# Kernel optimization log

Measured on AMD Instinct MI355X. Metric: run time of the kernel, lower is better.

The kernel has to match this reference:

```python
import jax, jax.numpy as jnp
import numpy as np

B, C, H, W = 2, 16, 128, 128
PS = (3, 5, 7)
N_BG, N_TG = 64, 8


def _unfold(x, p):
    # torch F.unfold(kernel=p, padding=p//2, stride=1): [B,C,H,W] -> [B, C*p*p, H*W]
    pad = p // 2
    b, c, h, w = x.shape
    xp = jnp.pad(x, ((0, 0), (0, 0), (pad, pad), (pad, pad)))
    # channel-major, then kernel row, kernel col (torch layout)
    pat = jnp.stack([xp[:, :, i:i + h, j:j + w] for i in range(p) for j in range(p)], axis=2)
    return pat.reshape(b, c * p * p, h * w)


def _fold(cols, p, h, w):
    # torch F.fold(output_size=(h,w), kernel=p, padding=p//2, stride=1): overlap-add scatter
    b, d, _ = cols.shape
    c = d // (p * p)
    pad = p // 2
    pat = cols.reshape(b, c, p * p, h, w)
    canvas = jnp.zeros((b, c, h + 2 * pad, w + 2 * pad), cols.dtype)
    for k in range(p * p):
        i, j = divmod(k, p)
        canvas = canvas.at[:, :, i:i + h, j:j + w].add(pat[:, :, k])
    return canvas[:, :, pad:pad + h, pad:pad + w]


def _branch(x, memory, temp, p):
    # _read_memory ('dot' similarity) + fold reconstruction with overlap-count divisor
    b, c, h, w = x.shape
    d = memory.shape[1]  # c*p*p
    xu = _unfold(x, p).transpose(0, 2, 1)                      # [B, HW, D]
    sim = jnp.einsum('bld,md->blm', xu, memory) * (temp[0] / d ** 0.5)
    att = jax.nn.softmax(sim, axis=2)                          # [B, HW, M]
    read = jnp.einsum('blm,md->bld', att, memory)              # [B, HW, D]
    out_sum = _fold(read.transpose(0, 2, 1), p, h, w)
    ones = jnp.ones((1, 1, h, w), x.dtype)
    div = _fold(_unfold(ones, p), p, h, w)                     # overlap counts
    return out_sum / (div + 1e-8)


def _fusion(feats, w1, b1, w2, b2):
    # MultiScaleFusion, fusion_type='attention'
    n = len(feats)
    b, c = feats[0].shape[0], feats[0].shape[1]
    u = feats[0]
    for f in feats[1:]:
        u = u + f
    pooled = u.mean(axis=(2, 3))                               # [B, C]
    hdn = jax.nn.relu(pooled @ w1.T + b1)                      # [B, C//4]
    logits = (hdn @ w2.T + b2).reshape(b, n, c)                # [B, n, C]
    wt = jax.nn.softmax(logits, axis=1)[..., None, None]       # softmax over scales
    return (jnp.stack(feats, axis=1) * wt).sum(axis=1)


def setup_inputs() -> dict:
    key = jax.random.key(0)
    ks = jax.random.split(key, 20)
    inp = {
        'bg': jax.random.normal(ks[0], (B, C, H, W), jnp.float32),
        'tg': jax.random.normal(ks[1], (B, C, H, W), jnp.float32),
    }
    for i, p in enumerate(PS):
        inp[f'bg_mem{i}'] = jax.random.normal(ks[2 + i], (N_BG, C * p * p), jnp.float32)
        inp[f'tg_mem{i}'] = jax.random.normal(ks[5 + i], (N_TG, C * p * p), jnp.float32)
        inp[f'bg_temp{i}'] = jnp.full((1,), 10.0, jnp.float32)
        inp[f'tg_temp{i}'] = jnp.full((1,), 10.0, jnp.float32)
    hid = C // 4
    n = len(PS)
    s1 = (1.0 / C) ** 0.5
    s2 = (1.0 / hid) ** 0.5
    inp['bg_fc1_w'] = jax.random.uniform(ks[8], (hid, C), jnp.float32, -s1, s1)
    inp['bg_fc1_b'] = jax.random.uniform(ks[9], (hid,), jnp.float32, -s1, s1)
    inp['bg_fc2_w'] = jax.random.uniform(ks[10], (C * n, hid), jnp.float32, -s2, s2)
    inp['bg_fc2_b'] = jax.random.uniform(ks[11], (C * n,), jnp.float32, -s2, s2)
    inp['tg_fc1_w'] = jax.random.uniform(ks[12], (hid, C), jnp.float32, -s1, s1)
    inp['tg_fc1_b'] = jax.random.uniform(ks[13], (hid,), jnp.float32, -s1, s1)
    inp['tg_fc2_w'] = jax.random.uniform(ks[14], (C * n, hid), jnp.float32, -s2, s2)
    inp['tg_fc2_b'] = jax.random.uniform(ks[15], (C * n,), jnp.float32, -s2, s2)
    return inp


def reference(bg, tg,
              bg_mem0, bg_mem1, bg_mem2, bg_temp0, bg_temp1, bg_temp2,
              tg_mem0, tg_mem1, tg_mem2, tg_temp0, tg_temp1, tg_temp2,
              bg_fc1_w, bg_fc1_b, bg_fc2_w, bg_fc2_b,
              tg_fc1_w, tg_fc1_b, tg_fc2_w, tg_fc2_b):
    bg_feats = [_branch(bg, m, t, p) for m, t, p in
                zip((bg_mem0, bg_mem1, bg_mem2), (bg_temp0, bg_temp1, bg_temp2), PS)]
    f_bc = _fusion(bg_feats, bg_fc1_w, bg_fc1_b, bg_fc2_w, bg_fc2_b)
    tg_feats = [_branch(tg, m, t, p) for m, t, p in
                zip((tg_mem0, tg_mem1, tg_mem2), (tg_temp0, tg_temp1, tg_temp2), PS)]
    f_tg = _fusion(tg_feats, tg_fc1_w, tg_fc1_b, tg_fc2_w, tg_fc2_b)
    return (f_bc, f_tg)
```

## Files before the change

kernel.cpp:

```cpp
#include <hip/hip_runtime.h>

#define C_CH 16
#define Hdim 128
#define Wdim 128
#define HWdim 16384
#define CHW (C_CH * HWdim)
#define Bdim 2
#define PAIR_ELEMS (Bdim * CHW)

#define XWP 140
#define XHP 140
#define XPL (XHP * XWP)

typedef float v2f __attribute__((ext_vector_type(2)));
typedef _Float16 h2 __attribute__((ext_vector_type(2)));
typedef _Float16 f16x8 __attribute__((ext_vector_type(8)));
typedef float f32x4 __attribute__((ext_vector_type(4)));

__device__ __forceinline__ unsigned pack2(float a, float b) {
  h2 h = {(_Float16)a, (_Float16)b};
  return __builtin_bit_cast(unsigned, h);
}
__device__ __forceinline__ void gadd(float* p, float v) {
  __hip_atomic_fetch_add(p, v, __ATOMIC_RELAXED, __HIP_MEMORY_SCOPE_AGENT);
}

struct PrepDesc {
  const float* mem;
  const float* temp;
  _Float16* simA;
  _Float16* readA;
  int M, D, P, tg;
};
struct PrepArgs { PrepDesc d[6]; };

__global__ __launch_bounds__(256) void k_preppad(PrepArgs a,
                                                 const float* __restrict__ bg,
                                                 const float* __restrict__ tg,
                                                 unsigned* __restrict__ xpad2)
{
  int bid = blockIdx.x;
  if (bid < 2048) {
    int idx = bid * 256 + threadIdx.x;
    int pp = idx >> 14;
    int hw = idx & (HWdim - 1);
    int y = hw >> 7, x = hw & 127;
    int z = pp >> 3, cp = pp & 7;
    const float* src = (z < 2) ? bg : tg;
    int b = z & 1;
    float av = src[((b * C_CH + 2 * cp) << 14) + hw];
    float bv = src[((b * C_CH + 2 * cp + 1) << 14) + hw];
    xpad2[(size_t)pp * XPL + (y + 6) * XWP + (x + 6)] = pack2(av, bv);
    return;
  }
  int p = bid - 2048;
  int gy = p / 196, gx = p - gy * 196;
  PrepDesc de = a.d[gy];
  int n = de.M * de.D;
  int idx = gx * 256 + threadIdx.x;
  if (idx >= n) return;
  int m = idx / de.D;
  int d = idx - m * de.D;
  float val = de.mem[idx];
  float sc = de.temp[0] / sqrtf((float)de.D);
  int pp = de.P * de.P;
  int c = d / pp;
  int r = d - c * pp;
  int i = r / de.P;
  int j = r - i * de.P;
  int uv = i * de.P + j;
  int uvp = uv >> 1, luv = uv & 1;
  int kk = luv * 16 + c, kg = kk >> 3, kl = kk & 7;
  int u = de.P - 1 - i, v = de.P - 1 - j;
  int uvf = u * de.P + v;
  float sv = val * sc;
  if (!de.tg) {
    int mt = m >> 4, row = m & 15;
    _Float16 hi = (_Float16)sv;
    size_t bi = ((size_t)uvp * 8 + mt) * 512 + row * 32 +
                (size_t)((kg ^ (row & 3)) * 8 + kl);
    de.simA[bi] = hi;
    de.simA[bi + 2048] = (_Float16)(sv - (float)hi);
    int ck = m >> 5, m5 = m & 31, kg2 = m5 >> 3, kl2 = m5 & 7;
    _Float16 hr = (_Float16)val;
    size_t b2 = (size_t)uvf * 2048 + (size_t)(ck * 2) * 512 + c * 32 +
                (size_t)((kg2 ^ (c & 3)) * 8 + kl2);
    de.readA[b2] = hr;
    de.readA[b2 + 512] = (_Float16)(val - (float)hr);
  } else {
    _Float16 hi = (_Float16)sv;
    size_t bi = (size_t)(uvp * 2) * 512 + m * 32 +
                (size_t)((kg ^ (m & 3)) * 8 + kl);
    de.simA[bi] = hi;
    de.simA[bi + 512] = (_Float16)(sv - (float)hi);
    int ch = uvf >> 2, q = uvf & 3;
    _Float16 hr = (_Float16)val;
    size_t b2 = (size_t)ch * 1024 + c * 32 +
                (size_t)((q ^ (c & 3)) * 8 + (m & 7));
    de.readA[b2] = hr;
    de.readA[b2 + 512] = (_Float16)(val - (float)hr);
  }
}

struct FusedArgs {
  const unsigned* xpad2;
  const _Float16* simA[3];
  const _Float16* readA[3];
  const _Float16* simAtg[3];
  const _Float16* readAtg[3];
  float* fbgs[3];
  float* ftgs[3];
  float* pooled;
};

#define SDB_OFF 17920
#define RBUF_OFF 40960
#define FX_SMEM 49152

template<int P, bool BG>
__device__ __forceinline__ void fused_body(
    const unsigned* __restrict__ xp,
    const _Float16* __restrict__ simA,
    const _Float16* __restrict__ readA,
    float* __restrict__ fout,
    float* __restrict__ poolp,
    unsigned char* smem, int tid, int x0, int y0)
{
  constexpr int PAD = P / 2;
  constexpr int THY = 8 + 2 * PAD, THX = 16 + 2 * PAD;
  constexpr int XH = 8 + 4 * PAD, XW = 16 + 4 * PAD;
  constexpr int NXP = XH * XW, NHP = THY * THX;
  constexpr int NT = (NHP + 15) / 16;
  constexpr int NUVP = (P * P + 1) / 2;
  constexpr int NCH = BG ? (P * P + 1) / 2 : (P * P + 3) / 4;
  constexpr int NMT = BG ? 4 : 1;
  constexpr int SCHB = BG ? 8192 : 2048;
  constexpr int RCHB = BG ? 8192 : 2048;
  constexpr int SLD = SCHB / 16, RLD = RCHB / 16;
  constexpr int NRACC = BG ? 4 : 2;

  unsigned char* xbuf = smem;
  unsigned char* att  = smem;
  unsigned char* sdb  = smem + SDB_OFF;
  unsigned char* rbuf = smem + RBUF_OFF;

  const int w = __builtin_amdgcn_readfirstlane(tid >> 6);
  const int lane = tid & 63;
  const int col = lane & 15, g = lane >> 4;

  const int oy = y0 - 2 * PAD + 6, ox = x0 - 2 * PAD + 6;
  for (int t = tid; t < 2 * NXP; t += 512) {
    int h = (t >= NXP) ? 1 : 0;
    int pix = t - h * NXP;
    int ly = pix / XW, lx = pix - ly * XW;
    const unsigned* s = xp + (size_t)(h * 4) * XPL + (oy + ly) * XWP + (ox + lx);
    uint4 vv = { s[0], s[XPL], s[2 * XPL], s[3 * XPL] };
    *(uint4*)(xbuf + (h * NXP + pix) * 16) = vv;
  }

  int ayv[3], axv[3];
#pragma unroll
  for (int ti = 0; ti < 3; ++ti) {
    int nt = w + ti * 8;
    int pix = nt * 16 + col;
    if (pix > NHP - 1) pix = NHP - 1;
    ayv[ti] = pix / THX;
    axv[ti] = pix - ayv[ti] * THX;
  }

  f32x4 acc[3][NMT];
#pragma unroll
  for (int ti = 0; ti < 3; ++ti)
#pragma unroll
    for (int mt = 0; mt < NMT; ++mt) acc[ti][mt] = (f32x4){0.f, 0.f, 0.f, 0.f};

  uint4 sreg;
  if (tid < SLD) sreg = *((const uint4*)simA + tid);
  for (int uvp = 0; uvp < NUVP; ++uvp) {
    if (tid < SLD) {
      *((uint4*)(sdb + (uvp & 1) * SCHB) + tid) = sreg;
      if (uvp + 1 < NUVP)
        sreg = *((const uint4*)(simA + (size_t)(uvp + 1) * (SCHB / 2)) + tid);
    }
    __syncthreads();

    const unsigned char* ab = sdb + (uvp & 1) * SCHB;
    f16x8 af[2][NMT];
#pragma unroll
    for (int s = 0; s < 2; ++s)
#pragma unroll
      for (int mt = 0; mt < NMT; ++mt)
        af[s][mt] = *(const f16x8*)(ab + (s * NMT + mt) * 1024 + col * 64 +
                                    ((g ^ (col & 3)) << 4));

    int uva = 2 * uvp;
    int uvb = uva + 1; if (uvb >= P * P) uvb = uva;
    const int ua = uva / P, va = uva - ua * P;
    const int ub = uvb / P, vb = uvb - ub * P;
    const int u_ = (g >= 2) ? ub : ua;
    const int v_ = (g >= 2) ? vb : va;

#pragma unroll
    for (int ti = 0; ti < 3; ++ti) {
      int nt = w + ti * 8;
      if (nt < NT) {
        int xpix = (ayv[ti] + u_) * XW + axv[ti] + v_;
        f16x8 bb = *(const f16x8*)(xbuf + ((g & 1) * NXP + xpix) * 16);
#pragma unroll
        for (int mt = 0; mt < NMT; ++mt) {
          acc[ti][mt] = __builtin_amdgcn_mfma_f32_16x16x32_f16(af[0][mt], bb, acc[ti][mt], 0, 0, 0);
          acc[ti][mt] = __builtin_amdgcn_mfma_f32_16x16x32_f16(af[1][mt], bb, acc[ti][mt], 0, 0, 0);
        }
      }
    }
  }

  uint4 rreg;
  if (tid < RLD) rreg = *((const uint4*)readA + tid);
  __syncthreads();

#pragma unroll
  for (int ti = 0; ti < 3; ++ti) {
    int nt = w + ti * 8;
    if (nt < NT) {
      int pa = nt * 16 + col;
      int say = pa / THX, sax = pa - say * THX;
      int gy = y0 + say - PAD, gx = x0 + sax - PAD;
      bool inimg = (pa < NHP) & (gy >= 0) & (gy < Hdim) & (gx >= 0) & (gx < Wdim);
      if constexpr (BG) {
        float l[16];
#pragma unroll
        for (int mt = 0; mt < 4; ++mt)
#pragma unroll
          for (int r = 0; r < 4; ++r) l[mt * 4 + r] = acc[ti][mt][r];
        float mx = l[0];
#pragma unroll
        for (int i2 = 1; i2 < 16; ++i2) mx = fmaxf(mx, l[i2]);
        mx = fmaxf(mx, __shfl_xor(mx, 16));
        mx = fmaxf(mx, __shfl_xor(mx, 32));
        float sum = 0.f;
#pragma unroll
        for (int i2 = 0; i2 < 16; ++i2) { l[i2] = __expf(l[i2] - mx); sum += l[i2]; }
        sum += __shfl_xor(sum, 16);
        sum += __shfl_xor(sum, 32);
        float inv = inimg ? (1.f / sum) : 0.f;
        unsigned char* base = att + pa * 128;
        int swz = (pa & 7) << 4;
#pragma unroll
        for (int mt = 0; mt < 4; ++mt) {
          uint2 st = { pack2(l[mt * 4 + 0] * inv, l[mt * 4 + 1] * inv),
                       pack2(l[mt * 4 + 2] * inv, l[mt * 4 + 3] * inv) };
          *(uint2*)(base + ((mt * 32 + g * 8) ^ swz)) = st;
        }
      } else {
        float l0 = acc[ti][0][0], l1 = acc[ti][0][1];
        float l2 = acc[ti][0][2], l3 = acc[ti][0][3];
        float mx = fmaxf(fmaxf(l0, l1), fmaxf(l2, l3));
        mx = fmaxf(mx, __shfl_xor(mx, 16));
        l0 = __expf(l0 - mx); l1 = __expf(l1 - mx);
        l2 = __expf(l2 - mx); l3 = __expf(l3 - mx);
        float sum = l0 + l1 + l2 + l3;
        sum += __shfl_xor(sum, 16);
        float inv = inimg ? (1.f / sum) : 0.f;
        if (g < 2) {
          uint2 st = { pack2(l0 * inv, l1 * inv), pack2(l2 * inv, l3 * inv) };
          *(uint2*)(att + pa * 16 + g * 8) = st;
        }
      }
    }
  }

  f32x4 racc[NRACC];
#pragma unroll
  for (int q = 0; q < NRACC; ++q) racc[q] = (f32x4){0.f, 0.f, 0.f, 0.f};

  for (int ch = 0; ch < NCH; ++ch) {
    __syncthreads();
    if (tid < RLD) {
      *((uint4*)rbuf + tid) = rreg;
      if (ch + 1 < NCH)
        rreg = *((const uint4*)(readA + (size_t)(ch + 1) * (RCHB / 2)) + tid);
    }
    __syncthreads();
    const unsigned char* ab = rbuf;
    if constexpr (BG) {
#pragma unroll
      for (int l = 0; l < 2; ++l) {
        int uv = 2 * ch + l;
        int uvc = (uv > P * P - 1) ? (P * P - 1) : uv;
        int u = uvc / P, v = uvc - u * P;
        int pix = (w + u) * THX + (col + v);
        int swz = (pix & 7) << 4;
#pragma unroll
        for (int ck = 0; ck < 2; ++ck) {
          f16x8 bb = *(const f16x8*)(att + pix * 128 + ((ck * 64 + g * 16) ^ swz));
          f16x8 ah = *(const f16x8*)(ab + (l * 4 + ck * 2 + 0) * 1024 + col * 64 +
                                     ((g ^ (col & 3)) << 4));
          f16x8 al = *(const f16x8*)(ab + (l * 4 + ck * 2 + 1) * 1024 + col * 64 +
                                     ((g ^ (col & 3)) << 4));
          racc[ck * 2 + 0] = __builtin_amdgcn_mfma_f32_16x16x32_f16(ah, bb, racc[ck * 2 + 0], 0, 0, 0);
          racc[ck * 2 + 1] = __builtin_amdgcn_mfma_f32_16x16x32_f16(al, bb, racc[ck * 2 + 1], 0, 0, 0);
        }
      }
    } else {
      int uv = 4 * ch + g;
      if (uv > P * P - 1) uv = P * P - 1;
      int u = uv / P, v = uv - u * P;
      int pix = (w + u) * THX + (col + v);
      f16x8 bb = *(const f16x8*)(att + pix * 16);
      int aoff = col * 64 + ((g ^ (col & 3)) << 4);
      f16x8 ah = *(const f16x8*)(ab + aoff);
      f16x8 al = *(const f16x8*)(ab + 1024 + aoff);
      racc[0] = __builtin_amdgcn_mfma_f32_16x16x32_f16(ah, bb, racc[0], 0, 0, 0);
      racc[1] = __builtin_amdgcn_mfma_f32_16x16x32_f16(al, bb, racc[1], 0, 0, 0);
    }
  }

  f32x4 sv;
  if constexpr (BG) sv = (racc[0] + racc[1]) + (racc[2] + racc[3]);
  else              sv = racc[0] + racc[1];
  int gy = y0 + w, gx = x0 + col;
  int cy = min(P - 1, gy + PAD) - max(0, gy + PAD - (Hdim - 1)) + 1;
  int cx = min(P - 1, gx + PAD) - max(0, gx + PAD - (Wdim - 1)) + 1;
  float inv = 1.f / ((float)(cy * cx) + 1e-8f);
  float o0 = sv[0] * inv, o1 = sv[1] * inv, o2 = sv[2] * inv, o3 = sv[3] * inv;
  float* outp = fout + (size_t)(g * 4) * HWdim + gy * Wdim + gx;
  outp[0] = o0;
  outp[(size_t)1 * HWdim] = o1;
  outp[(size_t)2 * HWdim] = o2;
  outp[(size_t)3 * HWdim] = o3;

  float s0 = o0, s1 = o1, s2 = o2, s3 = o3;
#pragma unroll
  for (int mask = 1; mask < 16; mask <<= 1) {
    s0 += __shfl_xor(s0, mask);
    s1 += __shfl_xor(s1, mask);
    s2 += __shfl_xor(s2, mask);
    s3 += __shfl_xor(s3, mask);
  }
  __syncthreads();
  float* red = (float*)rbuf;
  if (col == 0) {
    red[(w * 4 + g) * 4 + 0] = s0;
    red[(w * 4 + g) * 4 + 1] = s1;
    red[(w * 4 + g) * 4 + 2] = s2;
    red[(w * 4 + g) * 4 + 3] = s3;
  }
  __syncthreads();
  if (tid < 16) {
    float t = 0.f;
#pragma unroll
    for (int ww = 0; ww < 8; ++ww) t += red[ww * 16 + tid];
    gadd(poolp + tid, t * (1.0f / (float)HWdim));
  }
}

__global__ __launch_bounds__(512, 4) void k_fused(FusedArgs a) {
  __shared__ __align__(16) unsigned char smem[FX_SMEM];
  const int z = blockIdx.z;
  const int x0 = blockIdx.x * 16, y0 = blockIdx.y * 8;
  const int tid = threadIdx.x;
  if (z < 6) {
    const int si = z >> 1, b = z & 1;
    const unsigned* xp = a.xpad2 + (size_t)(b * 8) * XPL;
    float* pp = a.pooled + b * 16;
    if (si == 0)
      fused_body<7, true>(xp, a.simA[0], a.readA[0], a.fbgs[0] + (size_t)b * CHW, pp, smem, tid, x0, y0);
    else if (si == 1)
      fused_body<5, true>(xp, a.simA[1], a.readA[1], a.fbgs[1] + (size_t)b * CHW, pp, smem, tid, x0, y0);
    else
      fused_body<3, true>(xp, a.simA[2], a.readA[2], a.fbgs[2] + (size_t)b * CHW, pp, smem, tid, x0, y0);
  } else {
    const int zz = z - 6, si = zz >> 1, b = zz & 1;
    const unsigned* xp = a.xpad2 + (size_t)((2 + b) * 8) * XPL;
    float* pp = a.pooled + 32 + b * 16;
    if (si == 0)
      fused_body<7, false>(xp, a.simAtg[0], a.readAtg[0], a.ftgs[0] + (size_t)b * CHW, pp, smem, tid, x0, y0);
    else if (si == 1)
      fused_body<5, false>(xp, a.simAtg[1], a.readAtg[1], a.ftgs[1] + (size_t)b * CHW, pp, smem, tid, x0, y0);
    else
      fused_body<3, false>(xp, a.simAtg[2], a.readAtg[2], a.ftgs[2] + (size_t)b * CHW, pp, smem, tid, x0, y0);
  }
}

__global__ __launch_bounds__(256) void k_out(
    const float* __restrict__ fbg, const float* __restrict__ ftg,
    const float* __restrict__ pooled,
    const float* __restrict__ w1b, const float* __restrict__ b1b,
    const float* __restrict__ w2b, const float* __restrict__ b2b,
    const float* __restrict__ w1t, const float* __restrict__ b1t,
    const float* __restrict__ w2t, const float* __restrict__ b2t,
    float* __restrict__ out)
{
  __shared__ float hdn[2][2][4];
  __shared__ float lgs[2][2][48];
  __shared__ float swt[12][16];
  const int t = threadIdx.x;
  if (t < 16) {
    int br = t >> 3, b = (t >> 2) & 1, h = t & 3;
    const float* w1 = br ? w1t : w1b;
    const float* b1 = br ? b1t : b1b;
    float s = b1[h];
    for (int c = 0; c < C_CH; ++c) s += pooled[br * 32 + b * 16 + c] * w1[h * 16 + c];
    hdn[br][b][h] = fmaxf(s, 0.f);
  }
  __syncthreads();
  if (t < 192) {
    int br = t / 96, r = t - br * 96, b = r / 48, j = r - b * 48;
    const float* w2 = br ? w2t : w2b;
    const float* b2 = br ? b2t : b2b;
    float s = b2[j];
    for (int h = 0; h < 4; ++h) s += hdn[br][b][h] * w2[j * 4 + h];
    lgs[br][b][j] = s;
  }
  __syncthreads();
  if (t < 64) {
    int br = t >> 5, b = (t >> 4) & 1, c = t & 15;
    float l0 = lgs[br][b][c], l1 = lgs[br][b][16 + c], l2 = lgs[br][b][32 + c];
    float m = fmaxf(l0, fmaxf(l1, l2));
    float e0 = __expf(l0 - m), e1 = __expf(l1 - m), e2 = __expf(l2 - m);
    float inv = 1.f / (e0 + e1 + e2);
    swt[(br * 2 + b) * 3 + 0][c] = e0 * inv;
    swt[(br * 2 + b) * 3 + 1][c] = e1 * inv;
    swt[(br * 2 + b) * 3 + 2][c] = e2 * inv;
  }
  __syncthreads();

  int base = (blockIdx.x * 256 + t) * 4;
  int br  = base >> 19;
  int rem = base & ((1 << 19) - 1);
  int b   = rem >> 18;
  int off = rem & ((1 << 18) - 1);
  int c   = off >> 14;
  const float* f = (br == 0) ? fbg : ftg;
  int wb = (br * 2 + b) * 3;
  f32x4 acc = {0.f, 0.f, 0.f, 0.f};
#pragma unroll
  for (int s = 0; s < 3; ++s) {
    f32x4 v = *(const f32x4*)(f + (size_t)(s * 2 + b) * CHW + off);
    float wv = swt[wb + s][c];
    acc = __builtin_elementwise_fma((f32x4){wv, wv, wv, wv}, v, acc);
  }
  *(f32x4*)(out + base) = acc;
}

extern "C" void kernel_launch(void* const* d_in, const int* in_sizes, int n_in,
                              void* d_out, int out_size, void* d_ws, size_t ws_size,
                              hipStream_t stream)
{
  const float* bg = (const float*)d_in[0];
  const float* tg = (const float*)d_in[1];
  const float* bg_mem[3]  = {(const float*)d_in[2],  (const float*)d_in[6],  (const float*)d_in[10]};
  const float* tg_mem[3]  = {(const float*)d_in[3],  (const float*)d_in[7],  (const float*)d_in[11]};
  const float* bg_temp[3] = {(const float*)d_in[4],  (const float*)d_in[8],  (const float*)d_in[12]};
  const float* tg_temp[3] = {(const float*)d_in[5],  (const float*)d_in[9],  (const float*)d_in[13]};
  const float* bg_fc1_w = (const float*)d_in[14];
  const float* bg_fc1_b = (const float*)d_in[15];
  const float* bg_fc2_w = (const float*)d_in[16];
  const float* bg_fc2_b = (const float*)d_in[17];
  const float* tg_fc1_w = (const float*)d_in[18];
  const float* tg_fc1_b = (const float*)d_in[19];
  const float* tg_fc2_w = (const float*)d_in[20];
  const float* tg_fc2_b = (const float*)d_in[21];

  unsigned* ws = (unsigned*)d_ws;
  unsigned* xpad2   = ws;
  float*    pooled  = (float*)(ws + (size_t)32 * XPL);
  float*    wt      = pooled + 64;
  _Float16* simA    = (_Float16*)(wt + 192);
  _Float16* readA   = simA + 176128;
  _Float16* simAtg  = readA + 176128;
  _Float16* readAtg = simAtg + 44032;
  float*    ftg     = (float*)(readAtg + 23552);
  float*    fbg     = ftg + (size_t)6 * CHW;

  hipMemsetAsync(xpad2, 0, (size_t)837376 * 4, stream);

  const int   Ms[6] = {64, 64, 64, 8, 8, 8};
  const int   Ps[6] = {3, 5, 7, 3, 5, 7};
  const float* mems[6]  = {bg_mem[0], bg_mem[1], bg_mem[2], tg_mem[0], tg_mem[1], tg_mem[2]};
  const float* temps[6] = {bg_temp[0], bg_temp[1], bg_temp[2], tg_temp[0], tg_temp[1], tg_temp[2]};

  const size_t aOff[3]   = {0, 102400, 155648};
  const size_t sOffTg[3] = {0, 25600, 38912};
  const size_t rOffTg[3] = {0, 13312, 20480};

  PrepArgs pa;
  for (int k = 0; k < 6; ++k) {
    int D = C_CH * Ps[k] * Ps[k];
    int si = 2 - (k % 3);
    if (k < 3)
      pa.d[k] = {mems[k], temps[k], simA + aOff[si], readA + aOff[si],
                 Ms[k], D, Ps[k], 0};
    else
      pa.d[k] = {mems[k], temps[k], simAtg + sOffTg[si], readAtg + rOffTg[si],
                 Ms[k], D, Ps[k], 1};
  }
  k_preppad<<<3224, 256, 0, stream>>>(pa, bg, tg, xpad2);

  FusedArgs fa;
  fa.xpad2 = xpad2;
  fa.pooled = pooled;
  for (int si = 0; si < 3; ++si) {
    int p = 2 - si;
    fa.simA[si]    = simA + aOff[si];
    fa.readA[si]   = readA + aOff[si];
    fa.simAtg[si]  = simAtg + sOffTg[si];
    fa.readAtg[si] = readAtg + rOffTg[si];
    fa.fbgs[si]    = fbg + (size_t)p * 2 * CHW;
    fa.ftgs[si]    = ftg + (size_t)p * 2 * CHW;
  }

  k_fused<<<dim3(8, 16, 12), 512, 0, stream>>>(fa);

  k_out<<<1024, 256, 0, stream>>>(fbg, ftg, pooled,
                                  bg_fc1_w, bg_fc1_b, bg_fc2_w, bg_fc2_b,
                                  tg_fc1_w, tg_fc1_b, tg_fc2_w, tg_fc2_b,
                                  (float*)d_out);
}
```

Baseline: 173.1 us.

## Halve block size, read MFMA A-operands straight from global, drop LDS staging

The fused kernel now runs 256 threads per block instead of 512. Each wave covers more pixel tiles (5 similarity tiles, 2 output rows), so each A-fragment is reused across more MFMAs. The similarity and read weight matrices are no longer staged through LDS with double-buffered syncs. Each lane loads its A fragment directly from global/L2, with a register prefetch of the next chunk between hi and lo MFMA passes, and the prep kernel writes an unswizzled layout to match. This removes many __syncthreads and the LDS footprint for weights, but raises register pressure and global load traffic per wave.

```diff
diff --git a/kernel.cpp b/kernel.cpp
--- a/kernel.cpp
+++ b/kernel.cpp
@@ -70,33 +70,29 @@
   int j = r - i * de.P;
   int uv = i * de.P + j;
   int uvp = uv >> 1, luv = uv & 1;
-  int kk = luv * 16 + c, kg = kk >> 3, kl = kk & 7;
+  int kk = luv * 16 + c;
   int u = de.P - 1 - i, v = de.P - 1 - j;
   int uvf = u * de.P + v;
   float sv = val * sc;
   if (!de.tg) {
     int mt = m >> 4, row = m & 15;
     _Float16 hi = (_Float16)sv;
-    size_t bi = ((size_t)uvp * 8 + mt) * 512 + row * 32 +
-                (size_t)((kg ^ (row & 3)) * 8 + kl);
+    size_t bi = (size_t)uvp * 4096 + mt * 512 + row * 32 + kk;
     de.simA[bi] = hi;
     de.simA[bi + 2048] = (_Float16)(sv - (float)hi);
-    int ck = m >> 5, m5 = m & 31, kg2 = m5 >> 3, kl2 = m5 & 7;
+    int ck = m >> 5, m5 = m & 31;
     _Float16 hr = (_Float16)val;
-    size_t b2 = (size_t)uvf * 2048 + (size_t)(ck * 2) * 512 + c * 32 +
-                (size_t)((kg2 ^ (c & 3)) * 8 + kl2);
+    size_t b2 = (size_t)uvf * 2048 + ck * 1024 + c * 32 + m5;
     de.readA[b2] = hr;
     de.readA[b2 + 512] = (_Float16)(val - (float)hr);
   } else {
     _Float16 hi = (_Float16)sv;
-    size_t bi = (size_t)(uvp * 2) * 512 + m * 32 +
-                (size_t)((kg ^ (m & 3)) * 8 + kl);
+    size_t bi = (size_t)uvp * 1024 + m * 32 + kk;
     de.simA[bi] = hi;
     de.simA[bi + 512] = (_Float16)(sv - (float)hi);
     int ch = uvf >> 2, q = uvf & 3;
     _Float16 hr = (_Float16)val;
-    size_t b2 = (size_t)ch * 1024 + c * 32 +
-                (size_t)((q ^ (c & 3)) * 8 + (m & 7));
+    size_t b2 = (size_t)ch * 1024 + c * 32 + q * 8 + (m & 7);
     de.readA[b2] = hr;
     de.readA[b2 + 512] = (_Float16)(val - (float)hr);
   }
@@ -113,9 +109,8 @@
   float* pooled;
 };
 
-#define SDB_OFF 17920
-#define RBUF_OFF 40960
-#define FX_SMEM 49152
+#define PSCR_OFF 40960
+#define FX_SMEM 41472
 
 template<int P, bool BG>
 __device__ __forceinline__ void fused_body(
@@ -134,22 +129,21 @@
   constexpr int NUVP = (P * P + 1) / 2;
   constexpr int NCH = BG ? (P * P + 1) / 2 : (P * P + 3) / 4;
   constexpr int NMT = BG ? 4 : 1;
-  constexpr int SCHB = BG ? 8192 : 2048;
-  constexpr int RCHB = BG ? 8192 : 2048;
-  constexpr int SLD = SCHB / 16, RLD = RCHB / 16;
-  constexpr int NRACC = BG ? 4 : 2;
+  constexpr int SCHUNK = NMT * 2 * 1024;
+  constexpr int RCHUNK = BG ? 8192 : 2048;
+  constexpr int NTI = 5;
 
   unsigned char* xbuf = smem;
   unsigned char* att  = smem;
-  unsigned char* sdb  = smem + SDB_OFF;
-  unsigned char* rbuf = smem + RBUF_OFF;
+  float* pscr = (float*)(smem + PSCR_OFF);
 
   const int w = __builtin_amdgcn_readfirstlane(tid >> 6);
   const int lane = tid & 63;
   const int col = lane & 15, g = lane >> 4;
+  const int alo = col * 64 + g * 16;
 
   const int oy = y0 - 2 * PAD + 6, ox = x0 - 2 * PAD + 6;
-  for (int t = tid; t < 2 * NXP; t += 512) {
+  for (int t = tid; t < 2 * NXP; t += 256) {
     int h = (t >= NXP) ? 1 : 0;
     int pix = t - h * NXP;
     int ly = pix / XW, lx = pix - ly * XW;
@@ -158,40 +152,35 @@
     *(uint4*)(xbuf + (h * NXP + pix) * 16) = vv;
   }
 
-  int ayv[3], axv[3];
-#pragma unroll
-  for (int ti = 0; ti < 3; ++ti) {
-    int nt = w + ti * 8;
+  int ayv[NTI], axv[NTI];
+#pragma unroll
+  for (int ti = 0; ti < NTI; ++ti) {
+    int nt = w + ti * 4;
     int pix = nt * 16 + col;
     if (pix > NHP - 1) pix = NHP - 1;
     ayv[ti] = pix / THX;
     axv[ti] = pix - ayv[ti] * THX;
   }
 
-  f32x4 acc[3][NMT];
-#pragma unroll
-  for (int ti = 0; ti < 3; ++ti)
+  f32x4 acc[NTI][NMT];
+#pragma unroll
+  for (int ti = 0; ti < NTI; ++ti)
 #pragma unroll
     for (int mt = 0; mt < NMT; ++mt) acc[ti][mt] = (f32x4){0.f, 0.f, 0.f, 0.f};
 
-  uint4 sreg;
-  if (tid < SLD) sreg = *((const uint4*)simA + tid);
+  const unsigned char* sA = (const unsigned char*)simA;
+  f16x8 ah[NMT], al[NMT];
+#pragma unroll
+  for (int mt = 0; mt < NMT; ++mt)
+    ah[mt] = *(const f16x8*)(sA + mt * 1024 + alo);
+
+  __syncthreads();
+
   for (int uvp = 0; uvp < NUVP; ++uvp) {
-    if (tid < SLD) {
-      *((uint4*)(sdb + (uvp & 1) * SCHB) + tid) = sreg;
-      if (uvp + 1 < NUVP)
-        sreg = *((const uint4*)(simA + (size_t)(uvp + 1) * (SCHB / 2)) + tid);
-    }
-    __syncthreads();
-
-    const unsigned char* ab = sdb + (uvp & 1) * SCHB;
-    f16x8 af[2][NMT];
-#pragma unroll
-    for (int s = 0; s < 2; ++s)
-#pragma unroll
-      for (int mt = 0; mt < NMT; ++mt)
-        af[s][mt] = *(const f16x8*)(ab + (s * NMT + mt) * 1024 + col * 64 +
-                                    ((g ^ (col & 3)) << 4));
+    const unsigned char* cb = sA + (size_t)uvp * SCHUNK;
+#pragma unroll
+    for (int mt = 0; mt < NMT; ++mt)
+      al[mt] = *(const f16x8*)(cb + (NMT + mt) * 1024 + alo);
 
     int uva = 2 * uvp;
     int uvb = uva + 1; if (uvb >= P * P) uvb = uva;
@@ -200,28 +189,37 @@
     const int u_ = (g >= 2) ? ub : ua;
     const int v_ = (g >= 2) ? vb : va;
 
-#pragma unroll
-    for (int ti = 0; ti < 3; ++ti) {
-      int nt = w + ti * 8;
-      if (nt < NT) {
+    f16x8 bbv[NTI];
+#pragma unroll
+    for (int ti = 0; ti < NTI; ++ti) {
+      if (w + ti * 4 < NT) {
         int xpix = (ayv[ti] + u_) * XW + axv[ti] + v_;
-        f16x8 bb = *(const f16x8*)(xbuf + ((g & 1) * NXP + xpix) * 16);
-#pragma unroll
-        for (int mt = 0; mt < NMT; ++mt) {
-          acc[ti][mt] = __builtin_amdgcn_mfma_f32_16x16x32_f16(af[0][mt], bb, acc[ti][mt], 0, 0, 0);
-          acc[ti][mt] = __builtin_amdgcn_mfma_f32_16x16x32_f16(af[1][mt], bb, acc[ti][mt], 0, 0, 0);
-        }
+        bbv[ti] = *(const f16x8*)(xbuf + ((g & 1) * NXP + xpix) * 16);
+#pragma unroll
+        for (int mt = 0; mt < NMT; ++mt)
+          acc[ti][mt] = __builtin_amdgcn_mfma_f32_16x16x32_f16(ah[mt], bbv[ti], acc[ti][mt], 0, 0, 0);
       }
     }
-  }
-
-  uint4 rreg;
-  if (tid < RLD) rreg = *((const uint4*)readA + tid);
-  __syncthreads();
-
-#pragma unroll
-  for (int ti = 0; ti < 3; ++ti) {
-    int nt = w + ti * 8;
+    if (uvp + 1 < NUVP) {
+#pragma unroll
+      for (int mt = 0; mt < NMT; ++mt)
+        ah[mt] = *(const f16x8*)(cb + SCHUNK + mt * 1024 + alo);
+    }
+#pragma unroll
+    for (int ti = 0; ti < NTI; ++ti) {
+      if (w + ti * 4 < NT) {
+#pragma unroll
+        for (int mt = 0; mt < NMT; ++mt)
+          acc[ti][mt] = __builtin_amdgcn_mfma_f32_16x16x32_f16(al[mt], bbv[ti], acc[ti][mt], 0, 0, 0);
+      }
+    }
+  }
+
+  __syncthreads();
+
+#pragma unroll
+  for (int ti = 0; ti < NTI; ++ti) {
+    int nt = w + ti * 4;
     if (nt < NT) {
       int pa = nt * 16 + col;
       int say = pa / THX, sax = pa - say * THX;
@@ -269,93 +267,135 @@
       }
     }
   }
-
-  f32x4 racc[NRACC];
-#pragma unroll
-  for (int q = 0; q < NRACC; ++q) racc[q] = (f32x4){0.f, 0.f, 0.f, 0.f};
-
-  for (int ch = 0; ch < NCH; ++ch) {
-    __syncthreads();
-    if (tid < RLD) {
-      *((uint4*)rbuf + tid) = rreg;
-      if (ch + 1 < NCH)
-        rreg = *((const uint4*)(readA + (size_t)(ch + 1) * (RCHB / 2)) + tid);
-    }
-    __syncthreads();
-    const unsigned char* ab = rbuf;
-    if constexpr (BG) {
+  __syncthreads();
+
+  constexpr int NRC = BG ? 4 : 2;
+  f32x4 racc[2][NRC];
+#pragma unroll
+  for (int r = 0; r < 2; ++r)
+#pragma unroll
+    for (int q = 0; q < NRC; ++q) racc[r][q] = (f32x4){0.f, 0.f, 0.f, 0.f};
+
+  const unsigned char* rA = (const unsigned char*)readA;
+  if constexpr (BG) {
+    f16x8 rah[4];
+#pragma unroll
+    for (int l = 0; l < 2; ++l)
+#pragma unroll
+      for (int ck = 0; ck < 2; ++ck)
+        rah[l * 2 + ck] = *(const f16x8*)(rA + l * 4096 + ck * 2048 + alo);
+
+    for (int ch = 0; ch < NCH; ++ch) {
+      const unsigned char* cb = rA + (size_t)ch * RCHUNK;
+      f16x8 ral[4];
+#pragma unroll
+      for (int l = 0; l < 2; ++l)
+#pragma unroll
+        for (int ck = 0; ck < 2; ++ck)
+          ral[l * 2 + ck] = *(const f16x8*)(cb + l * 4096 + ck * 2048 + 1024 + alo);
+
+      f16x8 bbv[2][2][2];
 #pragma unroll
       for (int l = 0; l < 2; ++l) {
         int uv = 2 * ch + l;
-        int uvc = (uv > P * P - 1) ? (P * P - 1) : uv;
-        int u = uvc / P, v = uvc - u * P;
-        int pix = (w + u) * THX + (col + v);
-        int swz = (pix & 7) << 4;
-#pragma unroll
-        for (int ck = 0; ck < 2; ++ck) {
-          f16x8 bb = *(const f16x8*)(att + pix * 128 + ((ck * 64 + g * 16) ^ swz));
-          f16x8 ah = *(const f16x8*)(ab + (l * 4 + ck * 2 + 0) * 1024 + col * 64 +
-                                     ((g ^ (col & 3)) << 4));
-          f16x8 al = *(const f16x8*)(ab + (l * 4 + ck * 2 + 1) * 1024 + col * 64 +
-                                     ((g ^ (col & 3)) << 4));
-          racc[ck * 2 + 0] = __builtin_amdgcn_mfma_f32_16x16x32_f16(ah, bb, racc[ck * 2 + 0], 0, 0, 0);
-          racc[ck * 2 + 1] = __builtin_amdgcn_mfma_f32_16x16x32_f16(al, bb, racc[ck * 2 + 1], 0, 0, 0);
+        if (uv > P * P - 1) uv = P * P - 1;
+        int u = uv / P, v = uv - u * P;
+#pragma unroll
+        for (int r = 0; r < 2; ++r) {
+          int pix = (2 * w + r + u) * THX + (col + v);
+          int swz = (pix & 7) << 4;
+#pragma unroll
+          for (int ck = 0; ck < 2; ++ck)
+            bbv[l][r][ck] = *(const f16x8*)(att + pix * 128 + ((ck * 64 + g * 16) ^ swz));
         }
       }
-    } else {
+#pragma unroll
+      for (int l = 0; l < 2; ++l)
+#pragma unroll
+        for (int r = 0; r < 2; ++r)
+#pragma unroll
+          for (int ck = 0; ck < 2; ++ck)
+            racc[r][ck * 2 + 0] = __builtin_amdgcn_mfma_f32_16x16x32_f16(
+                rah[l * 2 + ck], bbv[l][r][ck], racc[r][ck * 2 + 0], 0, 0, 0);
+      if (ch + 1 < NCH) {
+#pragma unroll
+        for (int l = 0; l < 2; ++l)
+#pragma unroll
+          for (int ck = 0; ck < 2; ++ck)
+            rah[l * 2 + ck] = *(const f16x8*)(cb + RCHUNK + l * 4096 + ck * 2048 + alo);
+      }
+#pragma unroll
+      for (int l = 0; l < 2; ++l)
+#pragma unroll
+        for (int r = 0; r < 2; ++r)
+#pragma unroll
+          for (int ck = 0; ck < 2; ++ck)
+            racc[r][ck * 2 + 1] = __builtin_amdgcn_mfma_f32_16x16x32_f16(
+                ral[l * 2 + ck], bbv[l][r][ck], racc[r][ck * 2 + 1], 0, 0, 0);
+    }
+  } else {
+    f16x8 tah = *(const f16x8*)(rA + alo);
+    for (int ch = 0; ch < NCH; ++ch) {
+      const unsigned char* cb = rA + (size_t)ch * RCHUNK;
+      f16x8 tal = *(const f16x8*)(cb + 1024 + alo);
       int uv = 4 * ch + g;
       if (uv > P * P - 1) uv = P * P - 1;
       int u = uv / P, v = uv - u * P;
-      int pix = (w + u) * THX + (col + v);
-      f16x8 bb = *(const f16x8*)(att + pix * 16);
-      int aoff = col * 64 + ((g ^ (col & 3)) << 4);
-      f16x8 ah = *(const f16x8*)(ab + aoff);
-      f16x8 al = *(const f16x8*)(ab + 1024 + aoff);
-      racc[0] = __builtin_amdgcn_mfma_f32_16x16x32_f16(ah, bb, racc[0], 0, 0, 0);
-      racc[1] = __builtin_amdgcn_mfma_f32_16x16x32_f16(al, bb, racc[1], 0, 0, 0);
-    }
-  }
-
-  f32x4 sv;
-  if constexpr (BG) sv = (racc[0] + racc[1]) + (racc[2] + racc[3]);
-  else              sv = racc[0] + racc[1];
-  int gy = y0 + w, gx = x0 + col;
-  int cy = min(P - 1, gy + PAD) - max(0, gy + PAD - (Hdim - 1)) + 1;
-  int cx = min(P - 1, gx + PAD) - max(0, gx + PAD - (Wdim - 1)) + 1;
-  float inv = 1.f / ((float)(cy * cx) + 1e-8f);
-  float o0 = sv[0] * inv, o1 = sv[1] * inv, o2 = sv[2] * inv, o3 = sv[3] * inv;
-  float* outp = fout + (size_t)(g * 4) * HWdim + gy * Wdim + gx;
-  outp[0] = o0;
-  outp[(size_t)1 * HWdim] = o1;
-  outp[(size_t)2 * HWdim] = o2;
-  outp[(size_t)3 * HWdim] = o3;
-
-  float s0 = o0, s1 = o1, s2 = o2, s3 = o3;
-#pragma unroll
-  for (int mask = 1; mask < 16; mask <<= 1) {
-    s0 += __shfl_xor(s0, mask);
-    s1 += __shfl_xor(s1, mask);
-    s2 += __shfl_xor(s2, mask);
-    s3 += __shfl_xor(s3, mask);
-  }
-  __syncthreads();
-  float* red = (float*)rbuf;
-  if (col == 0) {
-    red[(w * 4 + g) * 4 + 0] = s0;
-    red[(w * 4 + g) * 4 + 1] = s1;
-    red[(w * 4 + g) * 4 + 2] = s2;
-    red[(w * 4 + g) * 4 + 3] = s3;
+      f16x8 bbt[2];
+#pragma unroll
+      for (int r = 0; r < 2; ++r) {
+        int pix = (2 * w + r + u) * THX + (col + v);
+        bbt[r] = *(const f16x8*)(att + pix * 16);
+      }
+#pragma unroll
+      for (int r = 0; r < 2; ++r)
+        racc[r][0] = __builtin_amdgcn_mfma_f32_16x16x32_f16(tah, bbt[r], racc[r][0], 0, 0, 0);
+      if (ch + 1 < NCH) tah = *(const f16x8*)(cb + RCHUNK + alo);
+#pragma unroll
+      for (int r = 0; r < 2; ++r)
+        racc[r][1] = __builtin_amdgcn_mfma_f32_16x16x32_f16(tal, bbt[r], racc[r][1], 0, 0, 0);
+    }
+  }
+
+#pragma unroll
+  for (int r = 0; r < 2; ++r) {
+    f32x4 sv;
+    if constexpr (BG) sv = (racc[r][0] + racc[r][1]) + (racc[r][2] + racc[r][3]);
+    else              sv = racc[r][0] + racc[r][1];
+    int gy = y0 + 2 * w + r, gx = x0 + col;
+    int cy = min(P - 1, gy + PAD) - max(0, gy + PAD - (Hdim - 1)) + 1;
+    int cx = min(P - 1, gx + PAD) - max(0, gx + PAD - (Wdim - 1)) + 1;
+    float inv = 1.f / ((float)(cy * cx) + 1e-8f);
+    float o0 = sv[0] * inv, o1 = sv[1] * inv, o2 = sv[2] * inv, o3 = sv[3] * inv;
+    float* outp = fout + (size_t)(g * 4) * HWdim + gy * Wdim + gx;
+    outp[0] = o0;
+    outp[(size_t)1 * HWdim] = o1;
+    outp[(size_t)2 * HWdim] = o2;
+    outp[(size_t)3 * HWdim] = o3;
+
+    float s0 = o0, s1 = o1, s2 = o2, s3 = o3;
+#pragma unroll
+    for (int mask = 1; mask < 16; mask <<= 1) {
+      s0 += __shfl_xor(s0, mask);
+      s1 += __shfl_xor(s1, mask);
+      s2 += __shfl_xor(s2, mask);
+      s3 += __shfl_xor(s3, mask);
+    }
+    if (col == 0) {
+      float* rp = pscr + ((2 * w + r) * 4 + g) * 4;
+      rp[0] = s0; rp[1] = s1; rp[2] = s2; rp[3] = s3;
+    }
   }
   __syncthreads();
   if (tid < 16) {
     float t = 0.f;
 #pragma unroll
-    for (int ww = 0; ww < 8; ++ww) t += red[ww * 16 + tid];
+    for (int ww = 0; ww < 8; ++ww) t += pscr[ww * 16 + tid];
     gadd(poolp + tid, t * (1.0f / (float)HWdim));
   }
 }
 
-__global__ __launch_bounds__(512, 4) void k_fused(FusedArgs a) {
+__global__ __launch_bounds__(256, 3) void k_fused(FusedArgs a) {
   __shared__ __align__(16) unsigned char smem[FX_SMEM];
   const int z = blockIdx.z;
   const int x0 = blockIdx.x * 16, y0 = blockIdx.y * 8;
@@ -511,7 +551,7 @@
     fa.ftgs[si]    = ftg + (size_t)p * 2 * CHW;
   }
 
-  k_fused<<<dim3(8, 16, 12), 512, 0, stream>>>(fa);
+  k_fused<<<dim3(8, 16, 12), 256, 0, stream>>>(fa);
 
   k_out<<<1024, 256, 0, stream>>>(fbg, ftg, pooled,
                                   bg_fc1_w, bg_fc1_b, bg_fc2_w, bg_fc2_b,
```

Result: slower. 201.0 us (+16.1%).

## Enlarge fused block tile to 16x16 outputs to cut halo recomputation

Applied to the files above, without the earlier changes.

The fused memory-read kernel now computes a 16x16 output tile per block instead of 16x8. Each wave handles two output rows, with four m-tiles in the similarity stage and two read-accumulator sets. This shrinks the fraction of halo pixels whose similarity and softmax are recomputed, and halves the block count. In exchange, LDS per block grows to about 71 KB and register use rises, which may lower occupancy. The grid also gets coarser, with fewer blocks per CU for load balancing.

```diff
diff --git a/kernel.cpp b/kernel.cpp
--- a/kernel.cpp
+++ b/kernel.cpp
@@ -113,9 +113,10 @@
   float* pooled;
 };
 
-#define SDB_OFF 17920
-#define RBUF_OFF 40960
-#define FX_SMEM 49152
+#define SDB_OFF 25088
+#define RBUF_OFF 63488
+#define PSCR_OFF 71680
+#define FX_SMEM 72704
 
 template<int P, bool BG>
 __device__ __forceinline__ void fused_body(
@@ -127,8 +128,8 @@
     unsigned char* smem, int tid, int x0, int y0)
 {
   constexpr int PAD = P / 2;
-  constexpr int THY = 8 + 2 * PAD, THX = 16 + 2 * PAD;
-  constexpr int XH = 8 + 4 * PAD, XW = 16 + 4 * PAD;
+  constexpr int THY = 16 + 2 * PAD, THX = 16 + 2 * PAD;
+  constexpr int XH = 16 + 4 * PAD, XW = 16 + 4 * PAD;
   constexpr int NXP = XH * XW, NHP = THY * THX;
   constexpr int NT = (NHP + 15) / 16;
   constexpr int NUVP = (P * P + 1) / 2;
@@ -138,11 +139,13 @@
   constexpr int RCHB = BG ? 8192 : 2048;
   constexpr int SLD = SCHB / 16, RLD = RCHB / 16;
   constexpr int NRACC = BG ? 4 : 2;
+  constexpr int NTI = 4;
 
   unsigned char* xbuf = smem;
   unsigned char* att  = smem;
   unsigned char* sdb  = smem + SDB_OFF;
   unsigned char* rbuf = smem + RBUF_OFF;
+  float* pscr = (float*)(smem + PSCR_OFF);
 
   const int w = __builtin_amdgcn_readfirstlane(tid >> 6);
   const int lane = tid & 63;
@@ -158,9 +161,9 @@
     *(uint4*)(xbuf + (h * NXP + pix) * 16) = vv;
   }
 
-  int ayv[3], axv[3];
-#pragma unroll
-  for (int ti = 0; ti < 3; ++ti) {
+  int ayv[NTI], axv[NTI];
+#pragma unroll
+  for (int ti = 0; ti < NTI; ++ti) {
     int nt = w + ti * 8;
     int pix = nt * 16 + col;
     if (pix > NHP - 1) pix = NHP - 1;
@@ -168,9 +171,9 @@
     axv[ti] = pix - ayv[ti] * THX;
   }
 
-  f32x4 acc[3][NMT];
-#pragma unroll
-  for (int ti = 0; ti < 3; ++ti)
+  f32x4 acc[NTI][NMT];
+#pragma unroll
+  for (int ti = 0; ti < NTI; ++ti)
 #pragma unroll
     for (int mt = 0; mt < NMT; ++mt) acc[ti][mt] = (f32x4){0.f, 0.f, 0.f, 0.f};
 
@@ -201,7 +204,7 @@
     const int v_ = (g >= 2) ? vb : va;
 
 #pragma unroll
-    for (int ti = 0; ti < 3; ++ti) {
+    for (int ti = 0; ti < NTI; ++ti) {
       int nt = w + ti * 8;
       if (nt < NT) {
         int xpix = (ayv[ti] + u_) * XW + axv[ti] + v_;
@@ -220,7 +223,7 @@
   __syncthreads();
 
 #pragma unroll
-  for (int ti = 0; ti < 3; ++ti) {
+  for (int ti = 0; ti < NTI; ++ti) {
     int nt = w + ti * 8;
     if (nt < NT) {
       int pa = nt * 16 + col;
@@ -270,9 +273,11 @@
     }
   }
 
-  f32x4 racc[NRACC];
-#pragma unroll
-  for (int q = 0; q < NRACC; ++q) racc[q] = (f32x4){0.f, 0.f, 0.f, 0.f};
+  f32x4 racc[2][NRACC];
+#pragma unroll
+  for (int r = 0; r < 2; ++r)
+#pragma unroll
+    for (int q = 0; q < NRACC; ++q) racc[r][q] = (f32x4){0.f, 0.f, 0.f, 0.f};
 
   for (int ch = 0; ch < NCH; ++ch) {
     __syncthreads();
@@ -289,68 +294,73 @@
         int uv = 2 * ch + l;
         int uvc = (uv > P * P - 1) ? (P * P - 1) : uv;
         int u = uvc / P, v = uvc - u * P;
-        int pix = (w + u) * THX + (col + v);
-        int swz = (pix & 7) << 4;
-#pragma unroll
-        for (int ck = 0; ck < 2; ++ck) {
-          f16x8 bb = *(const f16x8*)(att + pix * 128 + ((ck * 64 + g * 16) ^ swz));
-          f16x8 ah = *(const f16x8*)(ab + (l * 4 + ck * 2 + 0) * 1024 + col * 64 +
-                                     ((g ^ (col & 3)) << 4));
-          f16x8 al = *(const f16x8*)(ab + (l * 4 + ck * 2 + 1) * 1024 + col * 64 +
-                                     ((g ^ (col & 3)) << 4));
-          racc[ck * 2 + 0] = __builtin_amdgcn_mfma_f32_16x16x32_f16(ah, bb, racc[ck * 2 + 0], 0, 0, 0);
-          racc[ck * 2 + 1] = __builtin_amdgcn_mfma_f32_16x16x32_f16(al, bb, racc[ck * 2 + 1], 0, 0, 0);
+#pragma unroll
+        for (int r = 0; r < 2; ++r) {
+          int pix = (2 * w + r + u) * THX + (col + v);
+          int swz = (pix & 7) << 4;
+#pragma unroll
+          for (int ck = 0; ck < 2; ++ck) {
+            f16x8 bb = *(const f16x8*)(att + pix * 128 + ((ck * 64 + g * 16) ^ swz));
+            f16x8 ah = *(const f16x8*)(ab + (l * 4 + ck * 2 + 0) * 1024 + col * 64 +
+                                       ((g ^ (col & 3)) << 4));
+            f16x8 al = *(const f16x8*)(ab + (l * 4 + ck * 2 + 1) * 1024 + col * 64 +
+                                       ((g ^ (col & 3)) << 4));
+            racc[r][ck * 2 + 0] = __builtin_amdgcn_mfma_f32_16x16x32_f16(ah, bb, racc[r][ck * 2 + 0], 0, 0, 0);
+            racc[r][ck * 2 + 1] = __builtin_amdgcn_mfma_f32_16x16x32_f16(al, bb, racc[r][ck * 2 + 1], 0, 0, 0);
+          }
         }
       }
     } else {
       int uv = 4 * ch + g;
       if (uv > P * P - 1) uv = P * P - 1;
       int u = uv / P, v = uv - u * P;
-      int pix = (w + u) * THX + (col + v);
-      f16x8 bb = *(const f16x8*)(att + pix * 16);
       int aoff = col * 64 + ((g ^ (col & 3)) << 4);
       f16x8 ah = *(const f16x8*)(ab + aoff);
       f16x8 al = *(const f16x8*)(ab + 1024 + aoff);
-      racc[0] = __builtin_amdgcn_mfma_f32_16x16x32_f16(ah, bb, racc[0], 0, 0, 0);
-      racc[1] = __builtin_amdgcn_mfma_f32_16x16x32_f16(al, bb, racc[1], 0, 0, 0);
-    }
-  }
-
-  f32x4 sv;
-  if constexpr (BG) sv = (racc[0] + racc[1]) + (racc[2] + racc[3]);
-  else              sv = racc[0] + racc[1];
-  int gy = y0 + w, gx = x0 + col;
-  int cy = min(P - 1, gy + PAD) - max(0, gy + PAD - (Hdim - 1)) + 1;
-  int cx = min(P - 1, gx + PAD) - max(0, gx + PAD - (Wdim - 1)) + 1;
-  float inv = 1.f / ((float)(cy * cx) + 1e-8f);
-  float o0 = sv[0] * inv, o1 = sv[1] * inv, o2 = sv[2] * inv, o3 = sv[3] * inv;
-  float* outp = fout + (size_t)(g * 4) * HWdim + gy * Wdim + gx;
-  outp[0] = o0;
-  outp[(size_t)1 * HWdim] = o1;
-  outp[(size_t)2 * HWdim] = o2;
-  outp[(size_t)3 * HWdim] = o3;
-
-  float s0 = o0, s1 = o1, s2 = o2, s3 = o3;
-#pragma unroll
-  for (int mask = 1; mask < 16; mask <<= 1) {
-    s0 += __shfl_xor(s0, mask);
-    s1 += __shfl_xor(s1, mask);
-    s2 += __shfl_xor(s2, mask);
-    s3 += __shfl_xor(s3, mask);
-  }
-  __syncthreads();
-  float* red = (float*)rbuf;
-  if (col == 0) {
-    red[(w * 4 + g) * 4 + 0] = s0;
-    red[(w * 4 + g) * 4 + 1] = s1;
-    red[(w * 4 + g) * 4 + 2] = s2;
-    red[(w * 4 + g) * 4 + 3] = s3;
+#pragma unroll
+      for (int r = 0; r < 2; ++r) {
+        int pix = (2 * w + r + u) * THX + (col + v);
+        f16x8 bb = *(const f16x8*)(att + pix * 16);
+        racc[r][0] = __builtin_amdgcn_mfma_f32_16x16x32_f16(ah, bb, racc[r][0], 0, 0, 0);
+        racc[r][1] = __builtin_amdgcn_mfma_f32_16x16x32_f16(al, bb, racc[r][1], 0, 0, 0);
+      }
+    }
+  }
+
+#pragma unroll
+  for (int r = 0; r < 2; ++r) {
+    f32x4 sv;
+    if constexpr (BG) sv = (racc[r][0] + racc[r][1]) + (racc[r][2] + racc[r][3]);
+    else              sv = racc[r][0] + racc[r][1];
+    int gy = y0 + 2 * w + r, gx = x0 + col;
+    int cy = min(P - 1, gy + PAD) - max(0, gy + PAD - (Hdim - 1)) + 1;
+    int cx = min(P - 1, gx + PAD) - max(0, gx + PAD - (Wdim - 1)) + 1;
+    float inv = 1.f / ((float)(cy * cx) + 1e-8f);
+    float o0 = sv[0] * inv, o1 = sv[1] * inv, o2 = sv[2] * inv, o3 = sv[3] * inv;
+    float* outp = fout + (size_t)(g * 4) * HWdim + gy * Wdim + gx;
+    outp[0] = o0;
+    outp[(size_t)1 * HWdim] = o1;
+    outp[(size_t)2 * HWdim] = o2;
+    outp[(size_t)3 * HWdim] = o3;
+
+    float s0 = o0, s1 = o1, s2 = o2, s3 = o3;
+#pragma unroll
+    for (int mask = 1; mask < 16; mask <<= 1) {
+      s0 += __shfl_xor(s0, mask);
+      s1 += __shfl_xor(s1, mask);
+      s2 += __shfl_xor(s2, mask);
+      s3 += __shfl_xor(s3, mask);
+    }
+    if (col == 0) {
+      float* rp = pscr + ((2 * w + r) * 4 + g) * 4;
+      rp[0] = s0; rp[1] = s1; rp[2] = s2; rp[3] = s3;
+    }
   }
   __syncthreads();
   if (tid < 16) {
     float t = 0.f;
 #pragma unroll
-    for (int ww = 0; ww < 8; ++ww) t += red[ww * 16 + tid];
+    for (int ww = 0; ww < 16; ++ww) t += pscr[ww * 16 + tid];
     gadd(poolp + tid, t * (1.0f / (float)HWdim));
   }
 }
@@ -358,7 +368,7 @@
 __global__ __launch_bounds__(512, 4) void k_fused(FusedArgs a) {
   __shared__ __align__(16) unsigned char smem[FX_SMEM];
   const int z = blockIdx.z;
-  const int x0 = blockIdx.x * 16, y0 = blockIdx.y * 8;
+  const int x0 = blockIdx.x * 16, y0 = blockIdx.y * 16;
   const int tid = threadIdx.x;
   if (z < 6) {
     const int si = z >> 1, b = z & 1;
@@ -511,7 +521,7 @@
     fa.ftgs[si]    = ftg + (size_t)p * 2 * CHW;
   }
 
-  k_fused<<<dim3(8, 16, 12), 512, 0, stream>>>(fa);
+  k_fused<<<dim3(8, 8, 12), 512, 0, stream>>>(fa);
 
   k_out<<<1024, 256, 0, stream>>>(fbg, ftg, pooled,
                                   bg_fc1_w, bg_fc1_b, bg_fc2_w, bg_fc2_b,
```

Result: faster. 160.9 us (-7.0%).
